# Kernel optimization log

Measured on AMD Instinct MI355X. Metric: run time of the kernel, lower is better.

The kernel has to match this reference:

```python
import jax, jax.numpy as jnp
import numpy as np

B, T, H = 8, 512, 1024
DC = 8            # concept_dim_total = 6 + 2
DIN = H + DC      # 1032
V, L = 8, 4       # op_vocab_size, prog_len


def setup_inputs() -> dict:
    key = jax.random.key(0)
    ks = jax.random.split(key, 20)
    s = 0.02
    inp = {
        "x": jax.random.normal(ks[0], (B, T, H), dtype=jnp.float32),
        # concept classifier heads
        "W_tt": jax.random.normal(ks[1], (6, H), dtype=jnp.float32) * s,
        "b_tt": jnp.zeros((6,), jnp.float32),
        "W_pol": jax.random.normal(ks[2], (2, H), dtype=jnp.float32) * s,
        "b_pol": jnp.zeros((2,), jnp.float32),
        # program generator
        "W_c2h": jax.random.normal(ks[3], (H, DIN), dtype=jnp.float32) * s,
        "b_c2h": jnp.zeros((H,), jnp.float32),
        "W_ih": jax.random.normal(ks[4], (3 * H, DIN), dtype=jnp.float32) * s,
        "W_hh": jax.random.normal(ks[5], (3 * H, H), dtype=jnp.float32) * s,
        "b_ih": jnp.zeros((3 * H,), jnp.float32),
        "b_hh": jnp.zeros((3 * H,), jnp.float32),
        "W_proj": jax.random.normal(ks[6], (V, H), dtype=jnp.float32) * s,
        "b_proj": jnp.zeros((V,), jnp.float32),
        # op library: num_ops stacked Linear(DIN->H)-GELU-Linear(H->H)
        "W1": jax.random.normal(ks[7], (V, H, DIN), dtype=jnp.float32) * s,
        "b1": jnp.zeros((V, H), jnp.float32),
        "W2": jax.random.normal(ks[8], (V, H, H), dtype=jnp.float32) * s,
        "b2": jnp.zeros((V, H), jnp.float32),
    }
    return inp


def _forward(x, W_tt, b_tt, W_pol, b_pol, W_c2h, b_c2h, W_ih, W_hh, b_ih, b_hh,
             W_proj, b_proj, W1, b1, W2, b2):
    # concept classifier
    tt = x @ W_tt.T + b_tt              # (B,T,6)
    pol = x @ W_pol.T + b_pol           # (B,T,2)
    concept_feats = jnp.concatenate([tt, pol], axis=-1)  # (B,T,8)
    concept_summary = jnp.concatenate([tt.mean(axis=1), pol.mean(axis=1)], axis=-1)  # (B,8)
    pooled = x.mean(axis=1)             # (B,H)
    context = jnp.concatenate([pooled, concept_summary], axis=-1)  # (B,DIN)

    # program generator: GRU with zero inputs, h0 from context (PyTorch gate eqs)
    h0 = context @ W_c2h.T + b_c2h      # (B,H)
    zero_in = jnp.zeros((context.shape[0], DIN), x.dtype)
    gi = zero_in @ W_ih.T + b_ih        # (B,3H); zero-input contribution = bias
    gi_r, gi_z, gi_n = jnp.split(gi, 3, axis=-1)

    def gru_step(h, _):
        gh = h @ W_hh.T + b_hh
        gh_r, gh_z, gh_n = jnp.split(gh, 3, axis=-1)
        r = jax.nn.sigmoid(gi_r + gh_r)
        z = jax.nn.sigmoid(gi_z + gh_z)
        n = jnp.tanh(gi_n + r * gh_n)
        h_new = (1.0 - z) * n + z * h
        return h_new, h_new

    _, hs = jax.lax.scan(gru_step, h0, None, length=L)   # (L,B,H)
    rnn_out = jnp.transpose(hs, (1, 0, 2))               # (B,L,H)
    program_logits = rnn_out @ W_proj.T + b_proj         # (B,L,V)

    # op library: outputs are identical across L, so compute each op once and
    # average the softmax weights over L (exact same math as expand+mean).
    x_aug = jnp.concatenate([x, concept_feats], axis=-1)           # (B,T,DIN)
    hmid = jax.nn.gelu(jnp.einsum('btd,vhd->btvh', x_aug, W1) + b1, approximate=False)
    op_out = jnp.einsum('btvh,voh->btvo', hmid, W2) + b2           # (B,T,V,H)
    w = jax.nn.softmax(program_logits, axis=-1).mean(axis=1)       # (B,V)
    out = jnp.einsum('btvd,bv->btd', op_out, w)                    # (B,T,H)
    return out, program_logits, tt, pol, pooled


def reference(x, W_tt, b_tt, W_pol, b_pol, W_c2h, b_c2h, W_ih, W_hh, b_ih, b_hh,
              W_proj, b_proj, W1, b1, W2, b2):
    return _forward(x, W_tt, b_tt, W_pol, b_pol, W_c2h, b_c2h, W_ih, W_hh,
                    b_ih, b_hh, W_proj, b_proj, W1, b1, W2, b2)
```

## Files before the change

kernel.cpp:

```cpp
#include <hip/hip_runtime.h>
#include <hip/hip_bf16.h>
#include <math.h>

typedef __bf16 bf16;
typedef __bf16 bf16x8 __attribute__((ext_vector_type(8)));
typedef float f32x4 __attribute__((ext_vector_type(4)));


__device__ __forceinline__ float wsum(float v) {
#pragma unroll
  for (int off = 32; off; off >>= 1) v += __shfl_xor(v, off, 64);
  return v;
}

__device__ __forceinline__ void g2l16(const bf16* g, bf16* l) {
  __builtin_amdgcn_global_load_lds(
      (__attribute__((address_space(1))) void*)g,
      (__attribute__((address_space(3))) void*)l, 16, 0, 0);
}

__device__ __forceinline__ bf16x8 pack8(float4 a, float4 b) {
  bf16x8 r;
  r[0] = (bf16)a.x; r[1] = (bf16)a.y; r[2] = (bf16)a.z; r[3] = (bf16)a.w;
  r[4] = (bf16)b.x; r[5] = (bf16)b.y; r[6] = (bf16)b.z; r[7] = (bf16)b.w;
  return r;
}

__device__ __forceinline__ float gelu_fast(float x) {
  float s = __builtin_fabsf(x) * 0.70710678118654752f;
  float t = __builtin_amdgcn_rcpf(__builtin_fmaf(0.3275911f, s, 1.0f));
  float p = __builtin_fmaf(t, 1.061405429f, -1.453152027f);
  p = __builtin_fmaf(t, p, 1.421413741f);
  p = __builtin_fmaf(t, p, -0.284496736f);
  p = __builtin_fmaf(t, p, 0.254829592f);
  float e = exp2f(s * s * -1.4426950408889634f);
  float erf_abs = __builtin_fmaf(-p * t, e, 1.0f);
  return __builtin_fmaf(0.5f * __builtin_fabsf(x), erf_abs, 0.5f * x);
}

__global__ void k_cvt(const float* __restrict__ s, bf16* __restrict__ d, long n) {
  long stride = (long)gridDim.x * blockDim.x;
  for (long i = (long)blockIdx.x * blockDim.x + threadIdx.x; i * 8 < n; i += stride) {
    long e = i * 8;
    if (e + 8 <= n) {
      float4 a = *(const float4*)(s + e);
      float4 b = *(const float4*)(s + e + 4);
      *(bf16x8*)(d + e) = pack8(a, b);
    } else {
      for (long j = e; j < n; j++) d[j] = (bf16)s[j];
    }
  }
}

__global__ void k_xext(const float* __restrict__ x, const float* __restrict__ feats,
                       bf16* __restrict__ xbE, int H, int KE, int DC, long BT) {
  int wave = threadIdx.x >> 6, lane = threadIdx.x & 63;
  long m = (long)blockIdx.x * 4 + wave;
  if (m >= BT) return;
  const float* xp = x + m * H;
  bf16* dp = xbE + m * KE;
  for (int e = lane * 8; e + 8 <= H; e += 512) {
    float4 a = *(const float4*)(xp + e);
    float4 b = *(const float4*)(xp + e + 4);
    *(bf16x8*)(dp + e) = pack8(a, b);
  }
  int pad = KE - H;
  if (lane < pad)
    dp[H + lane] = (lane < DC) ? (bf16)feats[m * DC + lane] : (bf16)0.f;
}

__global__ void k_w1ext(const float* __restrict__ W1, bf16* __restrict__ W1bE,
                        int H, int DIN, int KE, int DC, long N2) {
  int wave = threadIdx.x >> 6, lane = threadIdx.x & 63;
  long n = (long)blockIdx.x * 4 + wave;
  if (n >= N2) return;
  const float* sp = W1 + n * DIN;
  bf16* dp = W1bE + n * KE;
  for (int e = lane * 8; e + 8 <= H; e += 512) {
    float4 a = *(const float4*)(sp + e);
    float4 b = *(const float4*)(sp + e + 4);
    *(bf16x8*)(dp + e) = pack8(a, b);
  }
  int pad = KE - H;
  if (lane < pad)
    dp[H + lane] = (lane < DC) ? (bf16)sp[H + lane] : (bf16)0.f;
}

template <int DCT>
__global__ void k_feats_t(const float* __restrict__ x,
                          const float* __restrict__ Wtt, const float* __restrict__ btt,
                          const float* __restrict__ Wpol, const float* __restrict__ bpol,
                          float* __restrict__ out_tt, float* __restrict__ out_pol,
                          float* __restrict__ feats,
                          int H, int T, int BT, int C1, int C2) {
  int wave = threadIdx.x >> 6, lane = threadIdx.x & 63;
  int site = blockIdx.x * 4 + wave;
  if (site >= BT) return;
  const float* xp = x + (size_t)site * H;
  const float* wp[DCT];
#pragma unroll
  for (int c = 0; c < DCT; c++)
    wp[c] = (c < C1) ? (Wtt + (size_t)c * H) : (Wpol + (size_t)(c - C1) * H);
  float acc[DCT];
#pragma unroll
  for (int c = 0; c < DCT; c++) acc[c] = 0.f;
  for (int k = lane * 4; k < H; k += 256) {
    float4 xv = *(const float4*)(xp + k);
#pragma unroll
    for (int c = 0; c < DCT; c++) {
      float4 wv4 = *(const float4*)(wp[c] + k);
      acc[c] += xv.x * wv4.x + xv.y * wv4.y + xv.z * wv4.z + xv.w * wv4.w;
    }
  }
#pragma unroll
  for (int c = 0; c < DCT; c++) acc[c] = wsum(acc[c]);
  if (lane == 0) {
#pragma unroll
    for (int c = 0; c < DCT; c++) {
      float val = acc[c] + (c < C1 ? btt[c] : bpol[c - C1]);
      if (c < C1) out_tt[(size_t)site * C1 + c] = val;
      else        out_pol[(size_t)site * C2 + (c - C1)] = val;
      feats[(size_t)site * DCT + c] = val;
    }
  }
}

__global__ void k_feats_g(const float* __restrict__ x,
                          const float* __restrict__ Wtt, const float* __restrict__ btt,
                          const float* __restrict__ Wpol, const float* __restrict__ bpol,
                          float* __restrict__ out_tt, float* __restrict__ out_pol,
                          float* __restrict__ feats,
                          int H, int T, int BT, int C1, int C2) {
  int wave = threadIdx.x >> 6, lane = threadIdx.x & 63;
  int site = blockIdx.x * 4 + wave;
  if (site >= BT) return;
  int DC = C1 + C2;
  const float* xp = x + (size_t)site * H;
  for (int c = 0; c < DC; c++) {
    const float* wr = (c < C1) ? (Wtt + (size_t)c * H) : (Wpol + (size_t)(c - C1) * H);
    float a = 0.f;
    for (int k = lane; k < H; k += 64) a += xp[k] * wr[k];
    a = wsum(a);
    if (lane == 0) {
      float val = a + (c < C1 ? btt[c] : bpol[c - C1]);
      if (c < C1) out_tt[(size_t)site * C1 + c] = val;
      else        out_pol[(size_t)site * C2 + (c - C1)] = val;
      feats[(size_t)site * DC + c] = val;
    }
  }
}

__global__ void k_fsum(const float* __restrict__ feats, float* __restrict__ fsum,
                       int T, int DC, int BDC) {
  int wave = threadIdx.x >> 6, lane = threadIdx.x & 63;
  int r = blockIdx.x * 4 + wave;
  if (r >= BDC) return;
  int b = r / DC, c = r % DC;
  const float* p = feats + ((size_t)b * T) * DC + c;
  float a = 0.f;
  for (int t = lane; t < T; t += 64) a += p[(size_t)t * DC];
  a = wsum(a);
  if (lane == 0) fsum[r] = a / (float)T;
}

__global__ void k_pool(const float* __restrict__ x, float* __restrict__ pooled,
                       int H, int T, int tsplit) {
  int hBlocks = (H + 255) / 256;
  int bs = blockIdx.x / tsplit, ts = blockIdx.x % tsplit;
  int b = bs / hBlocks;
  int h = (bs % hBlocks) * 256 + threadIdx.x;
  if (h >= H) return;
  int tlo = (int)(((long)T * ts) / tsplit), thi = (int)(((long)T * (ts + 1)) / tsplit);
  const float* p = x + (size_t)b * T * H + h;
  float s = 0.f;
  for (int t = tlo; t < thi; t++) s += p[(size_t)t * H];
  atomicAdd(&pooled[(size_t)b * H + h], s / (float)T);
}

__global__ void k_ctx_h0(const float* __restrict__ Wc2h, const float* __restrict__ bc2h,
                         const float* __restrict__ pooled, const float* __restrict__ fmean,
                         float* __restrict__ h0, float* __restrict__ out_pool,
                         int H, int DIN, int B, int DC) {
  int wave = threadIdx.x >> 6, lane = threadIdx.x & 63;
  int r = blockIdx.x * 4 + wave;
  if (r >= B * H) return;
  int b = r / H, j = r % H;
  const float* wrow = Wc2h + (size_t)j * DIN;
  float a = 0.f;
  for (int k = lane; k < DIN; k += 64) {
    float cv = (k < H) ? pooled[(size_t)b * H + k] : fmean[b * DC + (k - H)];
    a += cv * wrow[k];
  }
  a = wsum(a);
  if (lane == 0) {
    h0[r] = a + bc2h[j];
    out_pool[r] = pooled[r];
  }
}

__global__ void k_gru(const float* __restrict__ hin, const float* __restrict__ Whh,
                      const float* __restrict__ bih, const float* __restrict__ bhh,
                      float* __restrict__ hout, float* __restrict__ hsl,
                      int H, int B) {
  int wave = threadIdx.x >> 6, lane = threadIdx.x & 63;
  int r = blockIdx.x * 4 + wave;
  if (r >= B * H) return;
  int b = r / H, j = r % H;
  const float* h = hin + (size_t)b * H;
  const float* w0 = Whh + (size_t)j * H;
  const float* w1 = Whh + (size_t)(H + j) * H;
  const float* w2 = Whh + (size_t)(2 * H + j) * H;
  float ar = 0, az = 0, an = 0;
  for (int k = lane; k < H; k += 64) {
    float hv = h[k];
    ar += hv * w0[k];
    az += hv * w1[k];
    an += hv * w2[k];
  }
  ar = wsum(ar); az = wsum(az); an = wsum(an);
  if (lane == 0) {
    float ghr = ar + bhh[j];
    float ghz = az + bhh[H + j];
    float ghn = an + bhh[2 * H + j];
    float rg = 1.f / (1.f + expf(-(bih[j] + ghr)));
    float zg = 1.f / (1.f + expf(-(bih[H + j] + ghz)));
    float ng = tanhf(bih[2 * H + j] + rg * ghn);
    float hn = (1.f - zg) * ng + zg * h[j];
    hout[r] = hn;
    hsl[r] = hn;
  }
}

__global__ void k_logits(const float* __restrict__ hs, const float* __restrict__ Wproj,
                         const float* __restrict__ bproj, float* __restrict__ logits,
                         float* __restrict__ out_log, int H, int B, int L, int V) {
  int wave = threadIdx.x >> 6, lane = threadIdx.x & 63;
  int r = blockIdx.x * 4 + wave;
  if (r >= B * L * V) return;
  int b = r / (L * V), rem = r % (L * V), l = rem / V, u = rem % V;
  const float* h = hs + ((size_t)l * B + b) * H;
  const float* w = Wproj + (size_t)u * H;
  float a = 0.f;
  for (int k = lane; k < H; k += 64) a += h[k] * w[k];
  a = wsum(a);
  if (lane == 0) {
    a += bproj[u];
    int idx = (b * L + l) * V + u;
    logits[idx] = a;
    out_log[idx] = a;
  }
}

__global__ void k_wmix(const float* __restrict__ logits, const float* __restrict__ b2,
                       float* __restrict__ wv, float* __restrict__ wb2,
                       int B, int L, int V, int H) {
  __shared__ float sm[2048];
  __shared__ float wsh[512];
  int t = threadIdx.x;
  if (t < B * L) {
    const float* lg = logits + t * V;
    float mx = lg[0];
    for (int u = 1; u < V; u++) mx = fmaxf(mx, lg[u]);
    float s = 0.f;
    for (int u = 0; u < V; u++) s += expf(lg[u] - mx);
    for (int u = 0; u < V; u++) sm[t * V + u] = expf(lg[u] - mx) / s;
  }
  __syncthreads();
  if (t < B * V) {
    int b = t / V, u = t % V;
    float a = 0.f;
    for (int l = 0; l < L; l++) a += sm[(b * L + l) * V + u];
    a /= (float)L;
    wsh[t] = a;
    wv[t] = a;
  }
  __syncthreads();
  for (int idx = t; idx < B * H; idx += 256) {
    int b = idx / H, o = idx % H;
    float a = 0.f;
    for (int u = 0; u < V; u++) a += wsh[b * V + u] * b2[(size_t)u * H + o];
    wb2[idx] = a;
  }
}

__global__ __launch_bounds__(256, 2) void gemm1_mfma(
    const bf16* __restrict__ A, const bf16* __restrict__ Bb, bf16* __restrict__ hmid,
    const float* __restrict__ b1, const float* __restrict__ wv,
    int rows, long moff, int KE, int H, int N, int T, int V) {
  __shared__ __align__(16) bf16 As[128 * 64];
  __shared__ __align__(16) bf16 Bs[128 * 64];
  const int wave = threadIdx.x >> 6, lane = threadIdx.x & 63;
  int bx = blockIdx.x, by = blockIdx.y;
  if (gridDim.x == 64 && (gridDim.y & 3) == 0) {
    int f = by * 64 + bx;
    int xcd = f & 7, q = f >> 3;
    int cs = q >> 5, t = q & 31;
    bx = xcd * 8 + (t & 7);
    by = cs * 4 + (t >> 3);
  }
  const int m0 = by * 128, n0 = bx * 128;
  const int mw = (wave >> 1) * 64, nw = (wave & 1) * 64;
  const int rr = lane >> 3;
  const int srcOff = ((lane & 7) ^ rr) << 3;
  const int rA = lane & 15, q4 = lane >> 4;
  f32x4 acc[4][4];
#pragma unroll
  for (int i = 0; i < 4; i++)
#pragma unroll
    for (int j = 0; j < 4; j++) acc[i][j] = (f32x4){0.f, 0.f, 0.f, 0.f};

  int arow[4], brow[4];
#pragma unroll
  for (int t = 0; t < 4; ++t) {
    int r = wave * 32 + t * 8 + rr;
    arow[t] = (m0 + r < rows) ? (m0 + r) : (rows - 1);
    brow[t] = (n0 + r < N) ? (n0 + r) : (N - 1);
  }

  for (int k0 = 0; k0 < KE; k0 += 64) {
    __syncthreads();
#pragma unroll
    for (int t = 0; t < 4; ++t) {
      int c = wave * 4 + t;
      g2l16(A + (size_t)arow[t] * KE + k0 + srcOff, &As[c * 512]);
      g2l16(Bb + (size_t)brow[t] * KE + k0 + srcOff, &Bs[c * 512]);
    }
    __syncthreads();
#pragma unroll
    for (int kk = 0; kk < 2; ++kk) {
      bf16x8 af[4], bfr[4];
#pragma unroll
      for (int i = 0; i < 4; i++) {
        int row = mw + i * 16 + rA;
        af[i] = *(const bf16x8*)&As[row * 64 + ((((kk << 2) + q4) ^ (row & 7)) << 3)];
      }
#pragma unroll
      for (int j = 0; j < 4; j++) {
        int row = nw + j * 16 + rA;
        bfr[j] = *(const bf16x8*)&Bs[row * 64 + ((((kk << 2) + q4) ^ (row & 7)) << 3)];
      }
#pragma unroll
      for (int i = 0; i < 4; i++)
#pragma unroll
        for (int j = 0; j < 4; j++)
          acc[i][j] = __builtin_amdgcn_mfma_f32_16x16x32_bf16(af[i], bfr[j], acc[i][j], 0, 0, 0);
    }
  }

  int vj[4];
  float b1j[4];
#pragma unroll
  for (int j = 0; j < 4; j++) {
    int n = n0 + nw + j * 16 + rA;
    if (n >= N) n = N - 1;
    vj[j] = n / H;
    b1j[j] = b1[n];
  }
  int bBase = ((T & 127) == 0) ? (int)((moff + m0) / T) : -1;
  float wfac[4];
#pragma unroll
  for (int j = 0; j < 4; j++)
    wfac[j] = (bBase >= 0) ? wv[bBase * V + vj[j]] : 0.f;
#pragma unroll
  for (int i = 0; i < 4; i++) {
#pragma unroll
    for (int r = 0; r < 4; r++) {
      int m = m0 + mw + i * 16 + q4 * 4 + r;
      if (m >= rows) continue;
      long gm = moff + m;
      int bb = (bBase >= 0) ? bBase : (int)(gm / T);
#pragma unroll
      for (int j = 0; j < 4; j++) {
        int n = n0 + nw + j * 16 + rA;
        if (n >= N) continue;
        float val = gelu_fast(acc[i][j][r] + b1j[j]);
        float wf = (bBase >= 0) ? wfac[j] : wv[bb * V + vj[j]];
        hmid[(size_t)m * N + n] = (bf16)(val * wf);
      }
    }
  }
}

__global__ __launch_bounds__(256, 2) void gemm2_mfma(
    const bf16* __restrict__ A, const bf16* __restrict__ W2b, float* __restrict__ part,
    long partStride, int rows, int H, int K, int kchunk) {
  __shared__ __align__(16) bf16 As[128 * 64];
  __shared__ __align__(16) bf16 Bs[128 * 64];
  const int wave = threadIdx.x >> 6, lane = threadIdx.x & 63;
  int bx = blockIdx.x, by = blockIdx.y;
  if (gridDim.x == 8 && (gridDim.y & 31) == 0) {
    int f = by * 8 + bx;
    int xcd = f & 7, q = f >> 3;
    int cs = q >> 5, t = q & 31;
    bx = t & 7;
    by = (xcd + (cs << 3)) * 4 + (t >> 3);
  }
  const int m0 = by * 128, n0 = bx * 128;
  const int mw = (wave >> 1) * 64, nw = (wave & 1) * 64;
  const int rr = lane >> 3;
  const int srcOff = ((lane & 7) ^ rr) << 3;
  const int rA = lane & 15, q4 = lane >> 4;
  int kz0 = blockIdx.z * kchunk;
  int kz1 = kz0 + kchunk; if (kz1 > K) kz1 = K;
  if (kz0 >= K) return;
  f32x4 acc[4][4];
#pragma unroll
  for (int i = 0; i < 4; i++)
#pragma unroll
    for (int j = 0; j < 4; j++) acc[i][j] = (f32x4){0.f, 0.f, 0.f, 0.f};

  int arow[4], brow[4];
#pragma unroll
  for (int t = 0; t < 4; ++t) {
    int r = wave * 32 + t * 8 + rr;
    arow[t] = (m0 + r < rows) ? (m0 + r) : (rows - 1);
    brow[t] = (n0 + r < H) ? (n0 + r) : (H - 1);
  }

  int kv = kz0 / H, kh = kz0 % H;
  for (int k0 = kz0; k0 < kz1; k0 += 64) {
    const bf16* Bk = W2b + (size_t)kv * H * H + kh;
    __syncthreads();
#pragma unroll
    for (int t = 0; t < 4; ++t) {
      int c = wave * 4 + t;
      g2l16(A + (size_t)arow[t] * K + k0 + srcOff, &As[c * 512]);
      g2l16(Bk + (size_t)brow[t] * H + srcOff, &Bs[c * 512]);
    }
    __syncthreads();
#pragma unroll
    for (int kk = 0; kk < 2; ++kk) {
      bf16x8 af[4], bfr[4];
#pragma unroll
      for (int i = 0; i < 4; i++) {
        int row = mw + i * 16 + rA;
        af[i] = *(const bf16x8*)&As[row * 64 + ((((kk << 2) + q4) ^ (row & 7)) << 3)];
      }
#pragma unroll
      for (int j = 0; j < 4; j++) {
        int row = nw + j * 16 + rA;
        bfr[j] = *(const bf16x8*)&Bs[row * 64 + ((((kk << 2) + q4) ^ (row & 7)) << 3)];
      }
#pragma unroll
      for (int i = 0; i < 4; i++)
#pragma unroll
        for (int j = 0; j < 4; j++)
          acc[i][j] = __builtin_amdgcn_mfma_f32_16x16x32_bf16(af[i], bfr[j], acc[i][j], 0, 0, 0);
    }
    kh += 64;
    if (kh >= H) { kh = 0; kv++; }
  }

  float* pz = part + (size_t)blockIdx.z * partStride;
#pragma unroll
  for (int i = 0; i < 4; i++) {
#pragma unroll
    for (int r = 0; r < 4; r++) {
      int m = m0 + mw + i * 16 + q4 * 4 + r;
      if (m >= rows) continue;
#pragma unroll
      for (int j = 0; j < 4; j++) {
        int n = n0 + nw + j * 16 + rA;
        if (n >= H) continue;
        pz[(size_t)m * H + n] = acc[i][j][r];
      }
    }
  }
}

__global__ void k_red(const float* __restrict__ part, const float* __restrict__ wb2,
                      float* __restrict__ outY, long moff, int rows, long partStride,
                      int H, int T, int ZS) {
  int wave = threadIdx.x >> 6, lane = threadIdx.x & 63;
  long m = (long)blockIdx.x * 4 + wave;
  if (m >= rows) return;
  long gm = moff + m;
  int b = (int)(gm / T);
  const float* w = wb2 + (size_t)b * H;
  float* d = outY + (size_t)gm * H;
  for (int e = lane * 4; e + 4 <= H; e += 256) {
    float4 s = *(const float4*)(w + e);
    for (int z = 0; z < ZS; z++) {
      float4 p = *(const float4*)(part + (size_t)z * partStride + (size_t)m * H + e);
      s.x += p.x; s.y += p.y; s.z += p.z; s.w += p.w;
    }
    *(float4*)(d + e) = s;
  }
}

extern "C" void kernel_launch(void* const* d_in, const int* in_sizes, int n_in,
                              void* d_out, int out_size, void* d_ws, size_t ws_size,
                              hipStream_t stream) {
  const float* x      = (const float*)d_in[0];
  const float* W_tt   = (const float*)d_in[1];
  const float* b_tt   = (const float*)d_in[2];
  const float* W_pol  = (const float*)d_in[3];
  const float* b_pol  = (const float*)d_in[4];
  const float* W_c2h  = (const float*)d_in[5];
  const float* b_c2h  = (const float*)d_in[6];
  const float* W_hh   = (const float*)d_in[8];
  const float* b_ih   = (const float*)d_in[9];
  const float* b_hh   = (const float*)d_in[10];
  const float* W_proj = (const float*)d_in[11];
  const float* b_proj = (const float*)d_in[12];
  const float* W1     = (const float*)d_in[13];
  const float* b1     = (const float*)d_in[14];
  const float* W2     = (const float*)d_in[15];
  const float* b2     = (const float*)d_in[16];
  float* out = (float*)d_out;
  char* ws = (char*)d_ws;

  const int C1 = in_sizes[2];
  const int C2 = in_sizes[4];
  const int H  = in_sizes[1] / C1;
  const int DC = C1 + C2;
  const int DIN = H + DC;
  const int V  = in_sizes[12];
  const long BT = (long)in_sizes[0] / H;
  long R = (long)out_size - BT * (long)(H + DC);
  int B = 0, L = 0;
  for (int Lc = 1; Lc <= 32; ++Lc) {
    long den = (long)Lc * V + H;
    if (R % den == 0) {
      long Bc = R / den;
      if (Bc >= 1 && BT % Bc == 0) {
        if (B == 0 || Lc == 4) { B = (int)Bc; L = Lc; }
        if (Lc == 4) break;
      }
    }
  }
  if (B == 0) { B = 8; L = 4; }
  const int T = (int)(BT / B);
  const long N2 = (long)V * H;
  const int KE = H + 64;
  const int ZS = 4;

  size_t o = 0;
  auto alloc = [&](size_t bytes) { size_t r = o; o = (o + bytes + 255) & ~(size_t)255; return r; };
  float* feats  = (float*)(ws + alloc((size_t)BT * DC * 4));
  size_t off_pooled = alloc((size_t)B * H * 4);
  float* pooled = (float*)(ws + off_pooled);
  float* fsum   = (float*)(ws + alloc((size_t)B * DC * 4));
  float* hbuf   = (float*)(ws + alloc((size_t)2 * B * H * 4));
  float* hs     = (float*)(ws + alloc((size_t)L * B * H * 4));
  float* logits = (float*)(ws + alloc((size_t)B * L * V * 4));
  float* wv     = (float*)(ws + alloc((size_t)B * V * 4));
  float* wb2    = (float*)(ws + alloc((size_t)B * H * 4));
  bf16* xbE  = (bf16*)(ws + alloc((size_t)BT * KE * 2));
  bf16* W1bE = (bf16*)(ws + alloc((size_t)N2 * KE * 2));
  bf16* W2b  = (bf16*)(ws + alloc((size_t)N2 * H * 2));
  size_t off_hmid = alloc(0);
  long rowBytes = N2 * 2 + (long)ZS * H * 4;
  long avail = (long)ws_size - (long)off_hmid;
  long Mc = ((avail / rowBytes) / 128) * 128;
  long bt128 = ((BT + 127) / 128) * 128;
  if (Mc > bt128) Mc = bt128;
  if (Mc < 128) Mc = 128;
  bf16* hmid = (bf16*)(ws + off_hmid);
  float* part = (float*)(ws + off_hmid + (size_t)Mc * N2 * 2);
  long partStride = Mc * (long)H;

  float* out_y    = out;
  float* out_log  = out_y + (size_t)BT * H;
  float* out_tt   = out_log + (size_t)B * L * V;
  float* out_pol  = out_tt + (size_t)BT * C1;
  float* out_pool = out_pol + (size_t)BT * C2;

  hipMemsetAsync(ws + off_pooled, 0, (size_t)B * H * 4, stream);

  k_cvt<<<4096, 256, 0, stream>>>(W2, W2b, N2 * (long)H);
  if (DC == 8 && (H & 1023) == 0)
    k_feats_t<8><<<(int)((BT + 3) / 4), 256, 0, stream>>>(x, W_tt, b_tt, W_pol, b_pol,
                                                          out_tt, out_pol, feats,
                                                          H, T, (int)BT, C1, C2);
  else
    k_feats_g<<<(int)((BT + 3) / 4), 256, 0, stream>>>(x, W_tt, b_tt, W_pol, b_pol,
                                                       out_tt, out_pol, feats,
                                                       H, T, (int)BT, C1, C2);
  k_fsum<<<(B * DC + 3) / 4, 256, 0, stream>>>(feats, fsum, T, DC, B * DC);
  k_xext<<<(int)((BT + 3) / 4), 256, 0, stream>>>(x, feats, xbE, H, KE, DC, BT);
  k_w1ext<<<(int)((N2 + 3) / 4), 256, 0, stream>>>(W1, W1bE, H, DIN, KE, DC, N2);
  int hBlocks = (H + 255) / 256;
  k_pool<<<B * hBlocks * 8, 256, 0, stream>>>(x, pooled, H, T, 8);
  k_ctx_h0<<<(B * H + 3) / 4, 256, 0, stream>>>(W_c2h, b_c2h, pooled, fsum,
                                                hbuf, out_pool, H, DIN, B, DC);
  float* hA = hbuf;
  float* hB = hbuf + (size_t)B * H;
  for (int l = 0; l < L; ++l) {
    k_gru<<<(B * H + 3) / 4, 256, 0, stream>>>((l & 1) ? hB : hA, W_hh, b_ih, b_hh,
                                               (l & 1) ? hA : hB, hs + (size_t)l * B * H,
                                               H, B);
  }
  k_logits<<<(B * L * V + 3) / 4, 256, 0, stream>>>(hs, W_proj, b_proj, logits,
                                                    out_log, H, B, L, V);
  k_wmix<<<1, 256, 0, stream>>>(logits, b2, wv, wb2, B, L, V, H);

  int kchunk = (int)((((N2 / ZS) + 63) / 64) * 64);
  for (long moff = 0; moff < BT; moff += Mc) {
    int rows = (int)(((BT - moff) < Mc) ? (BT - moff) : Mc);
    dim3 g1((unsigned)((N2 + 127) / 128), (unsigned)((rows + 127) / 128));
    dim3 g2((unsigned)((H + 127) / 128), (unsigned)((rows + 127) / 128), ZS);
    gemm1_mfma<<<g1, 256, 0, stream>>>(xbE + (size_t)moff * KE, W1bE, hmid, b1, wv,
                                       rows, moff, KE, H, (int)N2, T, V);
    gemm2_mfma<<<g2, 256, 0, stream>>>(hmid, W2b, part, partStride,
                                       rows, H, (int)N2, kchunk);
    k_red<<<(int)((rows + 3) / 4), 256, 0, stream>>>(part, wb2, out_y, moff, rows,
                                                     partStride, H, T, ZS);
  }
}
```

Measured before the change: 462.9 us.

## Fuse front-end kernels, widen GEMM1 tile, drop split-K in GEMM2

The feature-projection and x-to-bf16 conversion are merged into one kernel, the W1/W2 conversions share one launch, and pooling and feature-mean sums share one launch, cutting launches and an extra pass over x. GEMM1 moves to a 128x256 tile with a new XCD remap and no occupancy hint. GEMM2 drops split-K and the separate reduction kernel, adds double-buffered LDS loads, and writes output plus bias directly. This avoids the partial-sum traffic but leaves fewer GEMM2 blocks, each doing a longer K loop.

```diff
diff --git a/kernel.cpp b/kernel.cpp
--- a/kernel.cpp
+++ b/kernel.cpp
@@ -38,91 +38,50 @@
   return __builtin_fmaf(0.5f * __builtin_fabsf(x), erf_abs, 0.5f * x);
 }
 
-__global__ void k_cvt(const float* __restrict__ s, bf16* __restrict__ d, long n) {
-  long stride = (long)gridDim.x * blockDim.x;
-  for (long i = (long)blockIdx.x * blockDim.x + threadIdx.x; i * 8 < n; i += stride) {
-    long e = i * 8;
-    if (e + 8 <= n) {
-      float4 a = *(const float4*)(s + e);
-      float4 b = *(const float4*)(s + e + 4);
-      *(bf16x8*)(d + e) = pack8(a, b);
-    } else {
-      for (long j = e; j < n; j++) d[j] = (bf16)s[j];
-    }
-  }
-}
-
-__global__ void k_xext(const float* __restrict__ x, const float* __restrict__ feats,
-                       bf16* __restrict__ xbE, int H, int KE, int DC, long BT) {
+template <int DCT>
+__global__ void k_front_t(const float* __restrict__ x,
+                          const float* __restrict__ Wtt, const float* __restrict__ btt,
+                          const float* __restrict__ Wpol, const float* __restrict__ bpol,
+                          float* __restrict__ out_tt, float* __restrict__ out_pol,
+                          float* __restrict__ feats, bf16* __restrict__ xbE,
+                          int H, int KE, long BT, int C1, int C2) {
   int wave = threadIdx.x >> 6, lane = threadIdx.x & 63;
   long m = (long)blockIdx.x * 4 + wave;
   if (m >= BT) return;
   const float* xp = x + m * H;
   bf16* dp = xbE + m * KE;
+  const float* wp[DCT];
+#pragma unroll
+  for (int c = 0; c < DCT; c++)
+    wp[c] = (c < C1) ? (Wtt + (size_t)c * H) : (Wpol + (size_t)(c - C1) * H);
+  float acc[DCT];
+#pragma unroll
+  for (int c = 0; c < DCT; c++) acc[c] = 0.f;
   for (int e = lane * 8; e + 8 <= H; e += 512) {
     float4 a = *(const float4*)(xp + e);
     float4 b = *(const float4*)(xp + e + 4);
     *(bf16x8*)(dp + e) = pack8(a, b);
+#pragma unroll
+    for (int c = 0; c < DCT; c++) {
+      float4 wa = *(const float4*)(wp[c] + e);
+      float4 wb = *(const float4*)(wp[c] + e + 4);
+      acc[c] += a.x * wa.x + a.y * wa.y + a.z * wa.z + a.w * wa.w +
+                b.x * wb.x + b.y * wb.y + b.z * wb.z + b.w * wb.w;
+    }
+  }
+#pragma unroll
+  for (int c = 0; c < DCT; c++) acc[c] = wsum(acc[c]);
+  float fv = 0.f;
+#pragma unroll
+  for (int c = 0; c < DCT; c++) fv = (lane == c) ? acc[c] : fv;
+  if (lane < DCT) {
+    fv += (lane < C1) ? btt[lane] : bpol[lane - C1];
+    if (lane < C1) out_tt[m * C1 + lane] = fv;
+    else           out_pol[m * C2 + (lane - C1)] = fv;
+    feats[m * DCT + lane] = fv;
   }
   int pad = KE - H;
-  if (lane < pad)
-    dp[H + lane] = (lane < DC) ? (bf16)feats[m * DC + lane] : (bf16)0.f;
-}
-
-__global__ void k_w1ext(const float* __restrict__ W1, bf16* __restrict__ W1bE,
-                        int H, int DIN, int KE, int DC, long N2) {
-  int wave = threadIdx.x >> 6, lane = threadIdx.x & 63;
-  long n = (long)blockIdx.x * 4 + wave;
-  if (n >= N2) return;
-  const float* sp = W1 + n * DIN;
-  bf16* dp = W1bE + n * KE;
-  for (int e = lane * 8; e + 8 <= H; e += 512) {
-    float4 a = *(const float4*)(sp + e);
-    float4 b = *(const float4*)(sp + e + 4);
-    *(bf16x8*)(dp + e) = pack8(a, b);
-  }
-  int pad = KE - H;
-  if (lane < pad)
-    dp[H + lane] = (lane < DC) ? (bf16)sp[H + lane] : (bf16)0.f;
-}
-
-template <int DCT>
-__global__ void k_feats_t(const float* __restrict__ x,
-                          const float* __restrict__ Wtt, const float* __restrict__ btt,
-                          const float* __restrict__ Wpol, const float* __restrict__ bpol,
-                          float* __restrict__ out_tt, float* __restrict__ out_pol,
-                          float* __restrict__ feats,
-                          int H, int T, int BT, int C1, int C2) {
-  int wave = threadIdx.x >> 6, lane = threadIdx.x & 63;
-  int site = blockIdx.x * 4 + wave;
-  if (site >= BT) return;
-  const float* xp = x + (size_t)site * H;
-  const float* wp[DCT];
-#pragma unroll
-  for (int c = 0; c < DCT; c++)
-    wp[c] = (c < C1) ? (Wtt + (size_t)c * H) : (Wpol + (size_t)(c - C1) * H);
-  float acc[DCT];
-#pragma unroll
-  for (int c = 0; c < DCT; c++) acc[c] = 0.f;
-  for (int k = lane * 4; k < H; k += 256) {
-    float4 xv = *(const float4*)(xp + k);
-#pragma unroll
-    for (int c = 0; c < DCT; c++) {
-      float4 wv4 = *(const float4*)(wp[c] + k);
-      acc[c] += xv.x * wv4.x + xv.y * wv4.y + xv.z * wv4.z + xv.w * wv4.w;
-    }
-  }
-#pragma unroll
-  for (int c = 0; c < DCT; c++) acc[c] = wsum(acc[c]);
-  if (lane == 0) {
-#pragma unroll
-    for (int c = 0; c < DCT; c++) {
-      float val = acc[c] + (c < C1 ? btt[c] : bpol[c - C1]);
-      if (c < C1) out_tt[(size_t)site * C1 + c] = val;
-      else        out_pol[(size_t)site * C2 + (c - C1)] = val;
-      feats[(size_t)site * DCT + c] = val;
-    }
-  }
+  if (lane < pad) dp[H + lane] = (lane < DCT) ? (bf16)fv : (bf16)0.f;
 }
 
 __global__ void k_feats_g(const float* __restrict__ x,
@@ -150,31 +109,81 @@
   }
 }
 
-__global__ void k_fsum(const float* __restrict__ feats, float* __restrict__ fsum,
-                       int T, int DC, int BDC) {
-  int wave = threadIdx.x >> 6, lane = threadIdx.x & 63;
-  int r = blockIdx.x * 4 + wave;
-  if (r >= BDC) return;
-  int b = r / DC, c = r % DC;
-  const float* p = feats + ((size_t)b * T) * DC + c;
-  float a = 0.f;
-  for (int t = lane; t < T; t += 64) a += p[(size_t)t * DC];
-  a = wsum(a);
-  if (lane == 0) fsum[r] = a / (float)T;
-}
-
-__global__ void k_pool(const float* __restrict__ x, float* __restrict__ pooled,
-                       int H, int T, int tsplit) {
-  int hBlocks = (H + 255) / 256;
-  int bs = blockIdx.x / tsplit, ts = blockIdx.x % tsplit;
-  int b = bs / hBlocks;
-  int h = (bs % hBlocks) * 256 + threadIdx.x;
-  if (h >= H) return;
-  int tlo = (int)(((long)T * ts) / tsplit), thi = (int)(((long)T * (ts + 1)) / tsplit);
-  const float* p = x + (size_t)b * T * H + h;
-  float s = 0.f;
-  for (int t = tlo; t < thi; t++) s += p[(size_t)t * H];
-  atomicAdd(&pooled[(size_t)b * H + h], s / (float)T);
+__global__ void k_xext(const float* __restrict__ x, const float* __restrict__ feats,
+                       bf16* __restrict__ xbE, int H, int KE, int DC, long BT) {
+  int wave = threadIdx.x >> 6, lane = threadIdx.x & 63;
+  long m = (long)blockIdx.x * 4 + wave;
+  if (m >= BT) return;
+  const float* xp = x + m * H;
+  bf16* dp = xbE + m * KE;
+  for (int e = lane * 8; e + 8 <= H; e += 512) {
+    float4 a = *(const float4*)(xp + e);
+    float4 b = *(const float4*)(xp + e + 4);
+    *(bf16x8*)(dp + e) = pack8(a, b);
+  }
+  int pad = KE - H;
+  if (lane < pad)
+    dp[H + lane] = (lane < DC) ? (bf16)feats[m * DC + lane] : (bf16)0.f;
+}
+
+__global__ void k_prep(const float* __restrict__ W1, bf16* __restrict__ W1bE,
+                       const float* __restrict__ W2, bf16* __restrict__ W2b,
+                       int H, int DIN, int KE, int DC, long N2, int nW1, long nCvtThreads) {
+  int wave = threadIdx.x >> 6, lane = threadIdx.x & 63;
+  if (blockIdx.x < (unsigned)nW1) {
+    long n = (long)blockIdx.x * 4 + wave;
+    if (n >= N2) return;
+    const float* sp = W1 + n * DIN;
+    bf16* dp = W1bE + n * KE;
+    for (int e = lane * 8; e + 8 <= H; e += 512) {
+      float4 a = *(const float4*)(sp + e);
+      float4 b = *(const float4*)(sp + e + 4);
+      *(bf16x8*)(dp + e) = pack8(a, b);
+    }
+    int pad = KE - H;
+    if (lane < pad)
+      dp[H + lane] = (lane < DC) ? (bf16)sp[H + lane] : (bf16)0.f;
+  } else {
+    long n = N2 * (long)H;
+    for (long i = (long)(blockIdx.x - nW1) * 256 + threadIdx.x; i * 8 < n;
+         i += nCvtThreads) {
+      long e = i * 8;
+      if (e + 8 <= n) {
+        float4 a = *(const float4*)(W2 + e);
+        float4 b = *(const float4*)(W2 + e + 4);
+        *(bf16x8*)(W2b + e) = pack8(a, b);
+      } else {
+        for (long j = e; j < n; j++) W2b[j] = (bf16)W2[j];
+      }
+    }
+  }
+}
+
+__global__ void k_stats(const float* __restrict__ x, float* __restrict__ pooled,
+                        const float* __restrict__ feats, float* __restrict__ fsum,
+                        int H, int T, int tsplit, int DC, int BDC, int poolBlocks) {
+  int wave = threadIdx.x >> 6, lane = threadIdx.x & 63;
+  if (blockIdx.x < (unsigned)poolBlocks) {
+    int hBlocks = (H + 255) / 256;
+    int bs = blockIdx.x / tsplit, ts = blockIdx.x % tsplit;
+    int b = bs / hBlocks;
+    int h = (bs % hBlocks) * 256 + threadIdx.x;
+    if (h >= H) return;
+    int tlo = (int)(((long)T * ts) / tsplit), thi = (int)(((long)T * (ts + 1)) / tsplit);
+    const float* p = x + (size_t)b * T * H + h;
+    float s = 0.f;
+    for (int t = tlo; t < thi; t++) s += p[(size_t)t * H];
+    atomicAdd(&pooled[(size_t)b * H + h], s / (float)T);
+  } else {
+    int r = (blockIdx.x - poolBlocks) * 4 + wave;
+    if (r >= BDC) return;
+    int b = r / DC, c = r % DC;
+    const float* p = feats + ((size_t)b * T) * DC + c;
+    float a = 0.f;
+    for (int t = lane; t < T; t += 64) a += p[(size_t)t * DC];
+    a = wsum(a);
+    if (lane == 0) fsum[r] = a / (float)T;
+  }
 }
 
 __global__ void k_ctx_h0(const float* __restrict__ Wc2h, const float* __restrict__ bc2h,
@@ -283,21 +292,113 @@
   }
 }
 
-__global__ __launch_bounds__(256, 2) void gemm1_mfma(
+__global__ __launch_bounds__(256) void gemm1_mfma(
     const bf16* __restrict__ A, const bf16* __restrict__ Bb, bf16* __restrict__ hmid,
     const float* __restrict__ b1, const float* __restrict__ wv,
     int rows, long moff, int KE, int H, int N, int T, int V) {
   __shared__ __align__(16) bf16 As[128 * 64];
-  __shared__ __align__(16) bf16 Bs[128 * 64];
+  __shared__ __align__(16) bf16 Bs[256 * 64];
   const int wave = threadIdx.x >> 6, lane = threadIdx.x & 63;
   int bx = blockIdx.x, by = blockIdx.y;
-  if (gridDim.x == 64 && (gridDim.y & 3) == 0) {
-    int f = by * 64 + bx;
+  if (gridDim.x == 32) {
+    int f = by * 32 + bx;
     int xcd = f & 7, q = f >> 3;
-    int cs = q >> 5, t = q & 31;
-    bx = xcd * 8 + (t & 7);
-    by = cs * 4 + (t >> 3);
-  }
+    bx = xcd * 4 + (q & 3);
+    by = q >> 2;
+  }
+  const int m0 = by * 128, n0 = bx * 256;
+  const int mw = (wave >> 1) * 64, nw = (wave & 1) * 128;
+  const int rr = lane >> 3;
+  const int srcOff = ((lane & 7) ^ rr) << 3;
+  const int rA = lane & 15, q4 = lane >> 4;
+  f32x4 acc[4][8];
+#pragma unroll
+  for (int i = 0; i < 4; i++)
+#pragma unroll
+    for (int j = 0; j < 8; j++) acc[i][j] = (f32x4){0.f, 0.f, 0.f, 0.f};
+
+  int arow[4], brow[8];
+#pragma unroll
+  for (int t = 0; t < 4; ++t) {
+    int r = (wave * 4 + t) * 8 + rr;
+    arow[t] = (m0 + r < rows) ? (m0 + r) : (rows - 1);
+  }
+#pragma unroll
+  for (int t = 0; t < 8; ++t) {
+    int r = (wave * 8 + t) * 8 + rr;
+    brow[t] = (n0 + r < N) ? (n0 + r) : (N - 1);
+  }
+
+  for (int k0 = 0; k0 < KE; k0 += 64) {
+    __syncthreads();
+#pragma unroll
+    for (int t = 0; t < 4; ++t)
+      g2l16(A + (size_t)arow[t] * KE + k0 + srcOff, &As[(wave * 4 + t) * 512]);
+#pragma unroll
+    for (int t = 0; t < 8; ++t)
+      g2l16(Bb + (size_t)brow[t] * KE + k0 + srcOff, &Bs[(wave * 8 + t) * 512]);
+    __syncthreads();
+#pragma unroll
+    for (int kk = 0; kk < 2; ++kk) {
+      bf16x8 af[4];
+#pragma unroll
+      for (int i = 0; i < 4; i++) {
+        int row = mw + i * 16 + rA;
+        af[i] = *(const bf16x8*)&As[row * 64 + ((((kk << 2) + q4) ^ (row & 7)) << 3)];
+      }
+#pragma unroll
+      for (int j = 0; j < 8; j++) {
+        int row = nw + j * 16 + rA;
+        bf16x8 bfr = *(const bf16x8*)&Bs[row * 64 + ((((kk << 2) + q4) ^ (row & 7)) << 3)];
+#pragma unroll
+        for (int i = 0; i < 4; i++)
+          acc[i][j] = __builtin_amdgcn_mfma_f32_16x16x32_bf16(af[i], bfr, acc[i][j], 0, 0, 0);
+      }
+    }
+  }
+
+  int vj[8];
+  float b1j[8];
+#pragma unroll
+  for (int j = 0; j < 8; j++) {
+    int n = n0 + nw + j * 16 + rA;
+    if (n >= N) n = N - 1;
+    vj[j] = n / H;
+    b1j[j] = b1[n];
+  }
+  int bBase = ((T & 127) == 0) ? (int)((moff + m0) / T) : -1;
+  float wfac[8];
+#pragma unroll
+  for (int j = 0; j < 8; j++)
+    wfac[j] = (bBase >= 0) ? wv[bBase * V + vj[j]] : 0.f;
+#pragma unroll
+  for (int i = 0; i < 4; i++) {
+#pragma unroll
+    for (int r = 0; r < 4; r++) {
+      int m = m0 + mw + i * 16 + q4 * 4 + r;
+      if (m >= rows) continue;
+      long gm = moff + m;
+      int bb = (bBase >= 0) ? bBase : (int)(gm / T);
+#pragma unroll
+      for (int j = 0; j < 8; j++) {
+        int n = n0 + nw + j * 16 + rA;
+        if (n >= N) continue;
+        float val = gelu_fast(acc[i][j][r] + b1j[j]);
+        float wf = (bBase >= 0) ? wfac[j] : wv[bb * V + vj[j]];
+        hmid[(size_t)m * N + n] = (bf16)(val * wf);
+      }
+    }
+  }
+}
+
+__global__ __launch_bounds__(256) void gemm2_mfma(
+    const bf16* __restrict__ A, const bf16* __restrict__ W2b,
+    const float* __restrict__ wb2, float* __restrict__ outY,
+    int rows, long moff, int H, int K, int T) {
+  __shared__ __align__(16) bf16 As[2][128 * 64];
+  __shared__ __align__(16) bf16 Bs[2][128 * 64];
+  const int wave = threadIdx.x >> 6, lane = threadIdx.x & 63;
+  const int bx = blockIdx.x, by = blockIdx.y;
   const int m0 = by * 128, n0 = bx * 128;
   const int mw = (wave >> 1) * 64, nw = (wave & 1) * 64;
   const int rr = lane >> 3;
@@ -312,32 +413,49 @@
   int arow[4], brow[4];
 #pragma unroll
   for (int t = 0; t < 4; ++t) {
-    int r = wave * 32 + t * 8 + rr;
+    int r = (wave * 4 + t) * 8 + rr;
     arow[t] = (m0 + r < rows) ? (m0 + r) : (rows - 1);
-    brow[t] = (n0 + r < N) ? (n0 + r) : (N - 1);
-  }
-
-  for (int k0 = 0; k0 < KE; k0 += 64) {
-    __syncthreads();
+    brow[t] = (n0 + r < H) ? (n0 + r) : (H - 1);
+  }
+
+  int k0s = 0, kvs = 0, khs = 0;
+  const int nt = K / 64;
+  {
+    const bf16* Bk = W2b + (size_t)kvs * H * H + khs;
 #pragma unroll
     for (int t = 0; t < 4; ++t) {
       int c = wave * 4 + t;
-      g2l16(A + (size_t)arow[t] * KE + k0 + srcOff, &As[c * 512]);
-      g2l16(Bb + (size_t)brow[t] * KE + k0 + srcOff, &Bs[c * 512]);
-    }
-    __syncthreads();
+      g2l16(A + (size_t)arow[t] * K + k0s + srcOff, &As[0][c * 512]);
+      g2l16(Bk + (size_t)brow[t] * H + srcOff, &Bs[0][c * 512]);
+    }
+    k0s += 64; khs += 64; if (khs >= H) { khs = 0; kvs++; }
+  }
+  __syncthreads();
+
+  int cur = 0;
+  for (int t = 0; t < nt; ++t) {
+    if (t + 1 < nt) {
+      const bf16* Bk = W2b + (size_t)kvs * H * H + khs;
+#pragma unroll
+      for (int s = 0; s < 4; ++s) {
+        int c = wave * 4 + s;
+        g2l16(A + (size_t)arow[s] * K + k0s + srcOff, &As[cur ^ 1][c * 512]);
+        g2l16(Bk + (size_t)brow[s] * H + srcOff, &Bs[cur ^ 1][c * 512]);
+      }
+      k0s += 64; khs += 64; if (khs >= H) { khs = 0; kvs++; }
+    }
 #pragma unroll
     for (int kk = 0; kk < 2; ++kk) {
       bf16x8 af[4], bfr[4];
 #pragma unroll
       for (int i = 0; i < 4; i++) {
         int row = mw + i * 16 + rA;
-        af[i] = *(const bf16x8*)&As[row * 64 + ((((kk << 2) + q4) ^ (row & 7)) << 3)];
+        af[i] = *(const bf16x8*)&As[cur][row * 64 + ((((kk << 2) + q4) ^ (row & 7)) << 3)];
       }
 #pragma unroll
       for (int j = 0; j < 4; j++) {
         int row = nw + j * 16 + rA;
-        bfr[j] = *(const bf16x8*)&Bs[row * 64 + ((((kk << 2) + q4) ^ (row & 7)) << 3)];
+        bfr[j] = *(const bf16x8*)&Bs[cur][row * 64 + ((((kk << 2) + q4) ^ (row & 7)) << 3)];
       }
 #pragma unroll
       for (int i = 0; i < 4; i++)
@@ -345,22 +463,11 @@
         for (int j = 0; j < 4; j++)
           acc[i][j] = __builtin_amdgcn_mfma_f32_16x16x32_bf16(af[i], bfr[j], acc[i][j], 0, 0, 0);
     }
-  }
-
-  int vj[4];
-  float b1j[4];
-#pragma unroll
-  for (int j = 0; j < 4; j++) {
-    int n = n0 + nw + j * 16 + rA;
-    if (n >= N) n = N - 1;
-    vj[j] = n / H;
-    b1j[j] = b1[n];
-  }
+    __syncthreads();
+    cur ^= 1;
+  }
+
   int bBase = ((T & 127) == 0) ? (int)((moff + m0) / T) : -1;
-  float wfac[4];
-#pragma unroll
-  for (int j = 0; j < 4; j++)
-    wfac[j] = (bBase >= 0) ? wv[bBase * V + vj[j]] : 0.f;
 #pragma unroll
   for (int i = 0; i < 4; i++) {
 #pragma unroll
@@ -369,122 +476,14 @@
       if (m >= rows) continue;
       long gm = moff + m;
       int bb = (bBase >= 0) ? bBase : (int)(gm / T);
-#pragma unroll
-      for (int j = 0; j < 4; j++) {
-        int n = n0 + nw + j * 16 + rA;
-        if (n >= N) continue;
-        float val = gelu_fast(acc[i][j][r] + b1j[j]);
-        float wf = (bBase >= 0) ? wfac[j] : wv[bb * V + vj[j]];
-        hmid[(size_t)m * N + n] = (bf16)(val * wf);
-      }
-    }
-  }
-}
-
-__global__ __launch_bounds__(256, 2) void gemm2_mfma(
-    const bf16* __restrict__ A, const bf16* __restrict__ W2b, float* __restrict__ part,
-    long partStride, int rows, int H, int K, int kchunk) {
-  __shared__ __align__(16) bf16 As[128 * 64];
-  __shared__ __align__(16) bf16 Bs[128 * 64];
-  const int wave = threadIdx.x >> 6, lane = threadIdx.x & 63;
-  int bx = blockIdx.x, by = blockIdx.y;
-  if (gridDim.x == 8 && (gridDim.y & 31) == 0) {
-    int f = by * 8 + bx;
-    int xcd = f & 7, q = f >> 3;
-    int cs = q >> 5, t = q & 31;
-    bx = t & 7;
-    by = (xcd + (cs << 3)) * 4 + (t >> 3);
-  }
-  const int m0 = by * 128, n0 = bx * 128;
-  const int mw = (wave >> 1) * 64, nw = (wave & 1) * 64;
-  const int rr = lane >> 3;
-  const int srcOff = ((lane & 7) ^ rr) << 3;
-  const int rA = lane & 15, q4 = lane >> 4;
-  int kz0 = blockIdx.z * kchunk;
-  int kz1 = kz0 + kchunk; if (kz1 > K) kz1 = K;
-  if (kz0 >= K) return;
-  f32x4 acc[4][4];
-#pragma unroll
-  for (int i = 0; i < 4; i++)
-#pragma unroll
-    for (int j = 0; j < 4; j++) acc[i][j] = (f32x4){0.f, 0.f, 0.f, 0.f};
-
-  int arow[4], brow[4];
-#pragma unroll
-  for (int t = 0; t < 4; ++t) {
-    int r = wave * 32 + t * 8 + rr;
-    arow[t] = (m0 + r < rows) ? (m0 + r) : (rows - 1);
-    brow[t] = (n0 + r < H) ? (n0 + r) : (H - 1);
-  }
-
-  int kv = kz0 / H, kh = kz0 % H;
-  for (int k0 = kz0; k0 < kz1; k0 += 64) {
-    const bf16* Bk = W2b + (size_t)kv * H * H + kh;
-    __syncthreads();
-#pragma unroll
-    for (int t = 0; t < 4; ++t) {
-      int c = wave * 4 + t;
-      g2l16(A + (size_t)arow[t] * K + k0 + srcOff, &As[c * 512]);
-      g2l16(Bk + (size_t)brow[t] * H + srcOff, &Bs[c * 512]);
-    }
-    __syncthreads();
-#pragma unroll
-    for (int kk = 0; kk < 2; ++kk) {
-      bf16x8 af[4], bfr[4];
-#pragma unroll
-      for (int i = 0; i < 4; i++) {
-        int row = mw + i * 16 + rA;
-        af[i] = *(const bf16x8*)&As[row * 64 + ((((kk << 2) + q4) ^ (row & 7)) << 3)];
-      }
-#pragma unroll
-      for (int j = 0; j < 4; j++) {
-        int row = nw + j * 16 + rA;
-        bfr[j] = *(const bf16x8*)&Bs[row * 64 + ((((kk << 2) + q4) ^ (row & 7)) << 3)];
-      }
-#pragma unroll
-      for (int i = 0; i < 4; i++)
-#pragma unroll
-        for (int j = 0; j < 4; j++)
-          acc[i][j] = __builtin_amdgcn_mfma_f32_16x16x32_bf16(af[i], bfr[j], acc[i][j], 0, 0, 0);
-    }
-    kh += 64;
-    if (kh >= H) { kh = 0; kv++; }
-  }
-
-  float* pz = part + (size_t)blockIdx.z * partStride;
-#pragma unroll
-  for (int i = 0; i < 4; i++) {
-#pragma unroll
-    for (int r = 0; r < 4; r++) {
-      int m = m0 + mw + i * 16 + q4 * 4 + r;
-      if (m >= rows) continue;
+      const float* wrow = wb2 + (size_t)bb * H;
 #pragma unroll
       for (int j = 0; j < 4; j++) {
         int n = n0 + nw + j * 16 + rA;
         if (n >= H) continue;
-        pz[(size_t)m * H + n] = acc[i][j][r];
-      }
-    }
-  }
-}
-
-__global__ void k_red(const float* __restrict__ part, const float* __restrict__ wb2,
-                      float* __restrict__ outY, long moff, int rows, long partStride,
-                      int H, int T, int ZS) {
-  int wave = threadIdx.x >> 6, lane = threadIdx.x & 63;
-  long m = (long)blockIdx.x * 4 + wave;
-  if (m >= rows) return;
-  long gm = moff + m;
-  int b = (int)(gm / T);
-  const float* w = wb2 + (size_t)b * H;
-  float* d = outY + (size_t)gm * H;
-  for (int e = lane * 4; e + 4 <= H; e += 256) {
-    float4 s = *(const float4*)(w + e);
-    for (int z = 0; z < ZS; z++) {
-      float4 p = *(const float4*)(part + (size_t)z * partStride + (size_t)m * H + e);
-      s.x += p.x; s.y += p.y; s.z += p.z; s.w += p.w;
-    }
-    *(float4*)(d + e) = s;
+        outY[(size_t)gm * H + n] = acc[i][j][r] + wrow[n];
+      }
+    }
   }
 }
 
@@ -533,7 +532,6 @@
   const int T = (int)(BT / B);
   const long N2 = (long)V * H;
   const int KE = H + 64;
-  const int ZS = 4;
 
   size_t o = 0;
   auto alloc = [&](size_t bytes) { size_t r = o; o = (o + bytes + 255) & ~(size_t)255; return r; };
@@ -550,15 +548,12 @@
   bf16* W1bE = (bf16*)(ws + alloc((size_t)N2 * KE * 2));
   bf16* W2b  = (bf16*)(ws + alloc((size_t)N2 * H * 2));
   size_t off_hmid = alloc(0);
-  long rowBytes = N2 * 2 + (long)ZS * H * 4;
   long avail = (long)ws_size - (long)off_hmid;
-  long Mc = ((avail / rowBytes) / 128) * 128;
+  long Mc = ((avail / (N2 * 2)) / 128) * 128;
   long bt128 = ((BT + 127) / 128) * 128;
   if (Mc > bt128) Mc = bt128;
   if (Mc < 128) Mc = 128;
   bf16* hmid = (bf16*)(ws + off_hmid);
-  float* part = (float*)(ws + off_hmid + (size_t)Mc * N2 * 2);
-  long partStride = Mc * (long)H;
 
   float* out_y    = out;
   float* out_log  = out_y + (size_t)BT * H;
@@ -568,20 +563,25 @@
 
   hipMemsetAsync(ws + off_pooled, 0, (size_t)B * H * 4, stream);
 
-  k_cvt<<<4096, 256, 0, stream>>>(W2, W2b, N2 * (long)H);
-  if (DC == 8 && (H & 1023) == 0)
-    k_feats_t<8><<<(int)((BT + 3) / 4), 256, 0, stream>>>(x, W_tt, b_tt, W_pol, b_pol,
-                                                          out_tt, out_pol, feats,
-                                                          H, T, (int)BT, C1, C2);
-  else
+  int nW1 = (int)((N2 + 3) / 4);
+  int nCvt = 1024;
+  k_prep<<<nW1 + nCvt, 256, 0, stream>>>(W1, W1bE, W2, W2b, H, DIN, KE, DC, N2,
+                                         nW1, (long)nCvt * 256);
+  if (DC == 8 && (H & 1023) == 0) {
+    k_front_t<8><<<(int)((BT + 3) / 4), 256, 0, stream>>>(x, W_tt, b_tt, W_pol, b_pol,
+                                                          out_tt, out_pol, feats, xbE,
+                                                          H, KE, BT, C1, C2);
+  } else {
     k_feats_g<<<(int)((BT + 3) / 4), 256, 0, stream>>>(x, W_tt, b_tt, W_pol, b_pol,
                                                        out_tt, out_pol, feats,
                                                        H, T, (int)BT, C1, C2);
-  k_fsum<<<(B * DC + 3) / 4, 256, 0, stream>>>(feats, fsum, T, DC, B * DC);
-  k_xext<<<(int)((BT + 3) / 4), 256, 0, stream>>>(x, feats, xbE, H, KE, DC, BT);
-  k_w1ext<<<(int)((N2 + 3) / 4), 256, 0, stream>>>(W1, W1bE, H, DIN, KE, DC, N2);
+    k_xext<<<(int)((BT + 3) / 4), 256, 0, stream>>>(x, feats, xbE, H, KE, DC, BT);
+  }
   int hBlocks = (H + 255) / 256;
-  k_pool<<<B * hBlocks * 8, 256, 0, stream>>>(x, pooled, H, T, 8);
+  int poolBlocks = B * hBlocks * 8;
+  int fsumBlocks = (B * DC + 3) / 4;
+  k_stats<<<poolBlocks + fsumBlocks, 256, 0, stream>>>(x, pooled, feats, fsum,
+                                                       H, T, 8, DC, B * DC, poolBlocks);
   k_ctx_h0<<<(B * H + 3) / 4, 256, 0, stream>>>(W_c2h, b_c2h, pooled, fsum,
                                                 hbuf, out_pool, H, DIN, B, DC);
   float* hA = hbuf;
@@ -595,16 +595,13 @@
                                                     out_log, H, B, L, V);
   k_wmix<<<1, 256, 0, stream>>>(logits, b2, wv, wb2, B, L, V, H);
 
-  int kchunk = (int)((((N2 / ZS) + 63) / 64) * 64);
   for (long moff = 0; moff < BT; moff += Mc) {
     int rows = (int)(((BT - moff) < Mc) ? (BT - moff) : Mc);
-    dim3 g1((unsigned)((N2 + 127) / 128), (unsigned)((rows + 127) / 128));
-    dim3 g2((unsigned)((H + 127) / 128), (unsigned)((rows + 127) / 128), ZS);
+    dim3 g1((unsigned)((N2 + 255) / 256), (unsigned)((rows + 127) / 128));
+    dim3 g2((unsigned)((H + 127) / 128), (unsigned)((rows + 127) / 128));
     gemm1_mfma<<<g1, 256, 0, stream>>>(xbE + (size_t)moff * KE, W1bE, hmid, b1, wv,
                                        rows, moff, KE, H, (int)N2, T, V);
-    gemm2_mfma<<<g2, 256, 0, stream>>>(hmid, W2b, part, partStride,
-                                       rows, H, (int)N2, kchunk);
-    k_red<<<(int)((rows + 3) / 4), 256, 0, stream>>>(part, wb2, out_y, moff, rows,
-                                                     partStride, H, T, ZS);
-  }
-}
+    gemm2_mfma<<<g2, 256, 0, stream>>>(hmid, W2b, wb2, out_y,
+                                       rows, moff, H, (int)N2, T);
+  }
+}
```

After: 648.4 us. 1.4x slower.
